# Optimization experiments

Hardware: AMD Instinct MI355X
Metric: run time of the kernel (lower is better)

The kernel has to match this reference:

```python
import jax, jax.numpy as jnp
import numpy as np

FILLER = 10.1  # filler_value from __init__
B, C, L, KEEP = 128, 16, 16384, 12288


def setup_inputs() -> dict:
    key = jax.random.key(0)
    k1, k2, k3, k4 = jax.random.split(key, 4)
    x1 = jax.random.normal(k1, (B, C, 4096), dtype=jnp.float32)
    x2 = jax.random.normal(k2, (B, C, 4096), dtype=jnp.float32)
    x3 = jax.random.normal(k3, (B, C, L), dtype=jnp.float32)
    # Scatter exactly (L - KEEP) filler entries at random positions in every row,
    # so per-row compaction yields a uniform length KEEP (required by np.stack
    # in the original module).
    u = jax.random.uniform(k4, (B, C, L))
    ranks = jnp.argsort(jnp.argsort(u, axis=-1), axis=-1)  # random permutation ranks
    fill_mask = ranks < (L - KEEP)
    x3 = jnp.where(fill_mask, jnp.float32(FILLER), x3)
    return {"x1": x1, "x2": x2, "x3": x3, "keep_len": KEEP}


def reference(x1, x2, x3, keep_len):
    # Per-row stream compaction: drop entries equal to FILLER, keep original
    # order of survivors, output fixed length keep_len.
    is_filler = x3 == jnp.float32(FILLER)          # [B, C, L] bool
    # Stable argsort moves non-filler (False=0) to the front, order-preserving.
    order = jnp.argsort(is_filler, axis=-1, stable=True)  # [B, C, L]
    compacted = jnp.take_along_axis(x3, order, axis=-1)    # [B, C, L]
    return compacted[..., :keep_len]                        # [B, C, keep_len]
```

## Files before the change

### kernel.cpp

```cpp
#include <hip/hip_runtime.h>


#define FILLER_VAL 10.1f
constexpr int L_LEN    = 16384;
constexpr int KEEP_LEN = 12288;
constexpr int BLOCK    = 256;
constexpr int NW       = BLOCK / 64;
constexpr int CHUNK    = BLOCK * 4;
constexpr int NC       = L_LEN / CHUNK;

__global__ __launch_bounds__(BLOCK) void compact_rows_kernel(
    const float* __restrict__ x3, float* __restrict__ out)
{
    const int row = blockIdx.x;
    const float* __restrict__ in = x3 + (size_t)row * L_LEN;
    float* __restrict__ o = out + (size_t)row * KEEP_LEN;

    const int tid  = threadIdx.x;
    const int lane = tid & 63;
    const int wid  = tid >> 6;
    const unsigned long long lt = (1ULL << lane) - 1ULL;

    __shared__ float stage[KEEP_LEN];
    __shared__ int wtot[NC][NW];

    float4 v[NC];
    #pragma unroll
    for (int c = 0; c < NC; ++c)
        v[c] = *reinterpret_cast<const float4*>(in + c * CHUNK + tid * 4);

    int before[NC];
    #pragma unroll
    for (int c = 0; c < NC; ++c) {
        unsigned long long m0 = __ballot(v[c].x != FILLER_VAL);
        unsigned long long m1 = __ballot(v[c].y != FILLER_VAL);
        unsigned long long m2 = __ballot(v[c].z != FILLER_VAL);
        unsigned long long m3 = __ballot(v[c].w != FILLER_VAL);
        before[c] = __popcll(m0 & lt) + __popcll(m1 & lt)
                  + __popcll(m2 & lt) + __popcll(m3 & lt);
        if (lane == 0)
            wtot[c][wid] = __popcll(m0) + __popcll(m1)
                         + __popcll(m2) + __popcll(m3);
    }
    __syncthreads();

    int run = 0;
    #pragma unroll
    for (int c = 0; c < NC; ++c) {
        int wb = run;
        #pragma unroll
        for (int w = 0; w < NW; ++w) {
            int t = wtot[c][w];
            if (w < wid) wb += t;
            run += t;
        }
        int pos = wb + before[c];
        if (v[c].x != FILLER_VAL) { if (pos < KEEP_LEN) stage[pos] = v[c].x; ++pos; }
        if (v[c].y != FILLER_VAL) { if (pos < KEEP_LEN) stage[pos] = v[c].y; ++pos; }
        if (v[c].z != FILLER_VAL) { if (pos < KEEP_LEN) stage[pos] = v[c].z; ++pos; }
        if (v[c].w != FILLER_VAL) { if (pos < KEEP_LEN) stage[pos] = v[c].w; ++pos; }
    }
    __syncthreads();

    #pragma unroll
    for (int k = 0; k < KEEP_LEN / (BLOCK * 4); ++k) {
        const int idx = (k * BLOCK + tid) * 4;
        float4 val = *reinterpret_cast<const float4*>(&stage[idx]);
        *reinterpret_cast<float4*>(&o[idx]) = val;
    }
}

extern "C" void kernel_launch(void* const* d_in, const int* in_sizes, int n_in,
                              void* d_out, int out_size, void* d_ws, size_t ws_size,
                              hipStream_t stream)
{
    const float* x3 = (const float*)d_in[2];
    float* out = (float*)d_out;

    const int rows = in_sizes[2] / L_LEN;

    compact_rows_kernel<<<rows, BLOCK, 0, stream>>>(x3, out);
}
```

Before: 256.4 us.

## Process two rows per 512-thread block with both rows' loads issued upfront

```diff
diff --git a/kernel.cpp b/kernel.cpp
--- a/kernel.cpp
+++ b/kernel.cpp
@@ -4,46 +4,47 @@
 #define FILLER_VAL 10.1f
 constexpr int L_LEN    = 16384;
 constexpr int KEEP_LEN = 12288;
-constexpr int BLOCK    = 256;
+constexpr int BLOCK    = 512;
 constexpr int NW       = BLOCK / 64;
 constexpr int CHUNK    = BLOCK * 4;
 constexpr int NC       = L_LEN / CHUNK;
 
-__global__ __launch_bounds__(BLOCK) void compact_rows_kernel(
-    const float* __restrict__ x3, float* __restrict__ out)
+struct RowState {
+    float4 v[NC];
+    int before[NC];
+    int b0[NC], b1[NC], b2[NC];
+};
+
+__device__ __forceinline__ void load_row(RowState& s, const float* __restrict__ in, int tid)
 {
-    const int row = blockIdx.x;
-    const float* __restrict__ in = x3 + (size_t)row * L_LEN;
-    float* __restrict__ o = out + (size_t)row * KEEP_LEN;
-
-    const int tid  = threadIdx.x;
-    const int lane = tid & 63;
-    const int wid  = tid >> 6;
-    const unsigned long long lt = (1ULL << lane) - 1ULL;
-
-    __shared__ float stage[KEEP_LEN];
-    __shared__ int wtot[NC][NW];
-
-    float4 v[NC];
     #pragma unroll
     for (int c = 0; c < NC; ++c)
-        v[c] = *reinterpret_cast<const float4*>(in + c * CHUNK + tid * 4);
+        s.v[c] = *reinterpret_cast<const float4*>(in + c * CHUNK + tid * 4);
+}
 
-    int before[NC];
+__device__ __forceinline__ void ballot_row(RowState& s, int lane, int wid,
+                                           unsigned long long lt, int (*wtot)[NW])
+{
     #pragma unroll
     for (int c = 0; c < NC; ++c) {
-        unsigned long long m0 = __ballot(v[c].x != FILLER_VAL);
-        unsigned long long m1 = __ballot(v[c].y != FILLER_VAL);
-        unsigned long long m2 = __ballot(v[c].z != FILLER_VAL);
-        unsigned long long m3 = __ballot(v[c].w != FILLER_VAL);
-        before[c] = __popcll(m0 & lt) + __popcll(m1 & lt)
-                  + __popcll(m2 & lt) + __popcll(m3 & lt);
+        unsigned long long m0 = __ballot(s.v[c].x != FILLER_VAL);
+        unsigned long long m1 = __ballot(s.v[c].y != FILLER_VAL);
+        unsigned long long m2 = __ballot(s.v[c].z != FILLER_VAL);
+        unsigned long long m3 = __ballot(s.v[c].w != FILLER_VAL);
+        s.before[c] = __popcll(m0 & lt) + __popcll(m1 & lt)
+                    + __popcll(m2 & lt) + __popcll(m3 & lt);
+        s.b0[c] = (int)((m0 >> lane) & 1ULL);
+        s.b1[c] = (int)((m1 >> lane) & 1ULL);
+        s.b2[c] = (int)((m2 >> lane) & 1ULL);
         if (lane == 0)
             wtot[c][wid] = __popcll(m0) + __popcll(m1)
                          + __popcll(m2) + __popcll(m3);
     }
-    __syncthreads();
+}
 
+__device__ __forceinline__ void scatter_row(const RowState& s, int wid,
+                                            float* stage, const int (*wtot)[NW])
+{
     int run = 0;
     #pragma unroll
     for (int c = 0; c < NC; ++c) {
@@ -54,20 +55,60 @@
             if (w < wid) wb += t;
             run += t;
         }
-        int pos = wb + before[c];
-        if (v[c].x != FILLER_VAL) { if (pos < KEEP_LEN) stage[pos] = v[c].x; ++pos; }
-        if (v[c].y != FILLER_VAL) { if (pos < KEEP_LEN) stage[pos] = v[c].y; ++pos; }
-        if (v[c].z != FILLER_VAL) { if (pos < KEEP_LEN) stage[pos] = v[c].z; ++pos; }
-        if (v[c].w != FILLER_VAL) { if (pos < KEEP_LEN) stage[pos] = v[c].w; ++pos; }
+        const int p0 = wb + s.before[c];
+        const int p1 = p0 + s.b0[c];
+        const int p2 = p1 + s.b1[c];
+        const int p3 = p2 + s.b2[c];
+        if (s.v[c].x != FILLER_VAL && p0 < KEEP_LEN) stage[p0] = s.v[c].x;
+        if (s.v[c].y != FILLER_VAL && p1 < KEEP_LEN) stage[p1] = s.v[c].y;
+        if (s.v[c].z != FILLER_VAL && p2 < KEEP_LEN) stage[p2] = s.v[c].z;
+        if (s.v[c].w != FILLER_VAL && p3 < KEEP_LEN) stage[p3] = s.v[c].w;
     }
-    __syncthreads();
+}
 
+__device__ __forceinline__ void copyout_row(const float* stage, float* __restrict__ o, int tid)
+{
     #pragma unroll
     for (int k = 0; k < KEEP_LEN / (BLOCK * 4); ++k) {
         const int idx = (k * BLOCK + tid) * 4;
-        float4 val = *reinterpret_cast<const float4*>(&stage[idx]);
-        *reinterpret_cast<float4*>(&o[idx]) = val;
+        *reinterpret_cast<float4*>(&o[idx]) =
+            *reinterpret_cast<const float4*>(&stage[idx]);
     }
+}
+
+__global__ __launch_bounds__(BLOCK, 6) void compact_rows_kernel(
+    const float* __restrict__ x3, float* __restrict__ out, int rows)
+{
+    const int row0 = blockIdx.x * 2;
+    const int row1 = row0 + 1;
+    const bool has1 = (row1 < rows);
+
+    const int tid  = threadIdx.x;
+    const int lane = tid & 63;
+    const int wid  = tid >> 6;
+    const unsigned long long lt = (1ULL << lane) - 1ULL;
+
+    __shared__ float stage[KEEP_LEN];
+    __shared__ int wtot[NC][NW];
+
+    RowState s0, s1;
+
+    load_row(s0, x3 + (size_t)row0 * L_LEN, tid);
+    if (has1) load_row(s1, x3 + (size_t)row1 * L_LEN, tid);
+
+    ballot_row(s0, lane, wid, lt, wtot);
+    __syncthreads();
+    scatter_row(s0, wid, stage, wtot);
+    __syncthreads();
+    copyout_row(stage, out + (size_t)row0 * KEEP_LEN, tid);
+
+    if (has1) ballot_row(s1, lane, wid, lt, wtot);
+    __syncthreads();
+    if (has1) {
+        scatter_row(s1, wid, stage, wtot);
+    }
+    __syncthreads();
+    if (has1) copyout_row(stage, out + (size_t)row1 * KEEP_LEN, tid);
 }
 
 extern "C" void kernel_launch(void* const* d_in, const int* in_sizes, int n_in,
@@ -78,6 +119,7 @@
     float* out = (float*)d_out;
 
     const int rows = in_sizes[2] / L_LEN;
+    const int grid = (rows + 1) / 2;
 
-    compact_rows_kernel<<<rows, BLOCK, 0, stream>>>(x3, out);
+    compact_rows_kernel<<<grid, BLOCK, 0, stream>>>(x3, out, rows);
 }
```

Measured after the change: 266.3 us. 3.9% more time.

## Stage 16-bit source indices in LDS and gather values from global memory

Applied to the files above, without the earlier changes.

```diff
diff --git a/kernel.cpp b/kernel.cpp
--- a/kernel.cpp
+++ b/kernel.cpp
@@ -9,7 +9,7 @@
 constexpr int CHUNK    = BLOCK * 4;
 constexpr int NC       = L_LEN / CHUNK;
 
-__global__ __launch_bounds__(BLOCK) void compact_rows_kernel(
+__global__ __launch_bounds__(BLOCK, 6) void compact_rows_kernel(
     const float* __restrict__ x3, float* __restrict__ out)
 {
     const int row = blockIdx.x;
@@ -21,23 +21,24 @@
     const int wid  = tid >> 6;
     const unsigned long long lt = (1ULL << lane) - 1ULL;
 
-    __shared__ float stage[KEEP_LEN];
+    __shared__ unsigned short stage[KEEP_LEN];
     __shared__ int wtot[NC][NW];
 
-    float4 v[NC];
-    #pragma unroll
-    for (int c = 0; c < NC; ++c)
-        v[c] = *reinterpret_cast<const float4*>(in + c * CHUNK + tid * 4);
-
-    int before[NC];
+    int pk[NC];
     #pragma unroll
     for (int c = 0; c < NC; ++c) {
-        unsigned long long m0 = __ballot(v[c].x != FILLER_VAL);
-        unsigned long long m1 = __ballot(v[c].y != FILLER_VAL);
-        unsigned long long m2 = __ballot(v[c].z != FILLER_VAL);
-        unsigned long long m3 = __ballot(v[c].w != FILLER_VAL);
-        before[c] = __popcll(m0 & lt) + __popcll(m1 & lt)
-                  + __popcll(m2 & lt) + __popcll(m3 & lt);
+        const float4 v = *reinterpret_cast<const float4*>(in + c * CHUNK + tid * 4);
+        const unsigned long long m0 = __ballot(v.x != FILLER_VAL);
+        const unsigned long long m1 = __ballot(v.y != FILLER_VAL);
+        const unsigned long long m2 = __ballot(v.z != FILLER_VAL);
+        const unsigned long long m3 = __ballot(v.w != FILLER_VAL);
+        const int before = __popcll(m0 & lt) + __popcll(m1 & lt)
+                         + __popcll(m2 & lt) + __popcll(m3 & lt);
+        const int bits = (int)((m0 >> lane) & 1ULL)
+                       | ((int)((m1 >> lane) & 1ULL) << 1)
+                       | ((int)((m2 >> lane) & 1ULL) << 2)
+                       | ((int)((m3 >> lane) & 1ULL) << 3);
+        pk[c] = bits | (before << 4);
         if (lane == 0)
             wtot[c][wid] = __popcll(m0) + __popcll(m1)
                          + __popcll(m2) + __popcll(m3);
@@ -50,23 +51,35 @@
         int wb = run;
         #pragma unroll
         for (int w = 0; w < NW; ++w) {
-            int t = wtot[c][w];
+            const int t = wtot[c][w];
             if (w < wid) wb += t;
             run += t;
         }
-        int pos = wb + before[c];
-        if (v[c].x != FILLER_VAL) { if (pos < KEEP_LEN) stage[pos] = v[c].x; ++pos; }
-        if (v[c].y != FILLER_VAL) { if (pos < KEEP_LEN) stage[pos] = v[c].y; ++pos; }
-        if (v[c].z != FILLER_VAL) { if (pos < KEEP_LEN) stage[pos] = v[c].z; ++pos; }
-        if (v[c].w != FILLER_VAL) { if (pos < KEEP_LEN) stage[pos] = v[c].w; ++pos; }
+        const int bits   = pk[c] & 15;
+        const int before = pk[c] >> 4;
+        const int p0 = wb + before;
+        const int p1 = p0 + (bits & 1);
+        const int p2 = p1 + ((bits >> 1) & 1);
+        const int p3 = p2 + ((bits >> 2) & 1);
+        const int idx = c * CHUNK + tid * 4;
+        if ((bits & 1) && p0 < KEEP_LEN) stage[p0] = (unsigned short)(idx);
+        if ((bits & 2) && p1 < KEEP_LEN) stage[p1] = (unsigned short)(idx + 1);
+        if ((bits & 4) && p2 < KEEP_LEN) stage[p2] = (unsigned short)(idx + 2);
+        if ((bits & 8) && p3 < KEEP_LEN) stage[p3] = (unsigned short)(idx + 3);
     }
     __syncthreads();
 
     #pragma unroll
-    for (int k = 0; k < KEEP_LEN / (BLOCK * 4); ++k) {
-        const int idx = (k * BLOCK + tid) * 4;
-        float4 val = *reinterpret_cast<const float4*>(&stage[idx]);
-        *reinterpret_cast<float4*>(&o[idx]) = val;
+    for (int it = 0; it < KEEP_LEN / (BLOCK * 8); ++it) {
+        const int o0 = it * (BLOCK * 8) + tid * 4;
+        const int o1 = o0 + BLOCK * 4;
+        const ushort4 i0 = *reinterpret_cast<const ushort4*>(&stage[o0]);
+        const ushort4 i1 = *reinterpret_cast<const ushort4*>(&stage[o1]);
+        float4 a, b;
+        a.x = in[i0.x]; a.y = in[i0.y]; a.z = in[i0.z]; a.w = in[i0.w];
+        b.x = in[i1.x]; b.y = in[i1.y]; b.z = in[i1.z]; b.w = in[i1.w];
+        *reinterpret_cast<float4*>(&o[o0]) = a;
+        *reinterpret_cast<float4*>(&o[o1]) = b;
     }
 }
 
```

New measurement: 272.0 us. 1.06x slower.

## Compact each row with a single wavefront using a streaming LDS ring buffer

Applied to the files above, without the earlier changes.

```diff
diff --git a/kernel.cpp b/kernel.cpp
--- a/kernel.cpp
+++ b/kernel.cpp
@@ -4,69 +4,87 @@
 #define FILLER_VAL 10.1f
 constexpr int L_LEN    = 16384;
 constexpr int KEEP_LEN = 12288;
-constexpr int BLOCK    = 256;
-constexpr int NW       = BLOCK / 64;
-constexpr int CHUNK    = BLOCK * 4;
-constexpr int NC       = L_LEN / CHUNK;
+constexpr int WAVE     = 64;
+constexpr int CHUNK    = WAVE * 4;
+constexpr int CPR      = L_LEN / CHUNK;
+constexpr int PF       = 8;
+constexpr int RING     = 2048;
+constexpr int RM       = RING - 1;
+constexpr int FLUSH_Q  = 256;
 
-__global__ __launch_bounds__(BLOCK) void compact_rows_kernel(
+__device__ __forceinline__ int lane_prefix(unsigned long long m)
+{
+    return __builtin_amdgcn_mbcnt_hi((unsigned)(m >> 32),
+           __builtin_amdgcn_mbcnt_lo((unsigned)m, 0u));
+}
+
+__global__ __launch_bounds__(WAVE, 4) void compact_rows_kernel(
     const float* __restrict__ x3, float* __restrict__ out)
 {
-    const int row = blockIdx.x;
+    const int row  = blockIdx.x;
+    const int lane = threadIdx.x;
     const float* __restrict__ in = x3 + (size_t)row * L_LEN;
     float* __restrict__ o = out + (size_t)row * KEEP_LEN;
 
-    const int tid  = threadIdx.x;
-    const int lane = tid & 63;
-    const int wid  = tid >> 6;
-    const unsigned long long lt = (1ULL << lane) - 1ULL;
+    __shared__ float ring[RING];
 
-    __shared__ float stage[KEEP_LEN];
-    __shared__ int wtot[NC][NW];
+    float4 buf[PF];
+    #pragma unroll
+    for (int i = 0; i < PF; ++i)
+        buf[i] = *reinterpret_cast<const float4*>(in + i * CHUNK + lane * 4);
 
-    float4 v[NC];
+    int rowoff  = 0;
+    int flushed = 0;
+
+    #pragma unroll 1
+    for (int g = 0; g < CPR / PF; ++g) {
+        #pragma unroll
+        for (int s = 0; s < PF; ++s) {
+            const int c = g * PF + s;
+            const float4 v = buf[s];
+            if (c + PF < CPR)
+                buf[s] = *reinterpret_cast<const float4*>(
+                    in + (c + PF) * CHUNK + lane * 4);
+
+            const bool kx = (v.x != FILLER_VAL);
+            const bool ky = (v.y != FILLER_VAL);
+            const bool kz = (v.z != FILLER_VAL);
+            const bool kw = (v.w != FILLER_VAL);
+            const unsigned long long m0 = __ballot(kx);
+            const unsigned long long m1 = __ballot(ky);
+            const unsigned long long m2 = __ballot(kz);
+            const unsigned long long m3 = __ballot(kw);
+
+            const int before = lane_prefix(m0) + lane_prefix(m1)
+                             + lane_prefix(m2) + lane_prefix(m3);
+            const int p0 = rowoff + before;
+            const int p1 = p0 + (int)kx;
+            const int p2 = p1 + (int)ky;
+            const int p3 = p2 + (int)kz;
+            if (kx) ring[p0 & RM] = v.x;
+            if (ky) ring[p1 & RM] = v.y;
+            if (kz) ring[p2 & RM] = v.z;
+            if (kw) ring[p3 & RM] = v.w;
+
+            rowoff += __popcll(m0) + __popcll(m1)
+                    + __popcll(m2) + __popcll(m3);
+
+            while (rowoff - flushed >= FLUSH_Q) {
+                const int rbase = (flushed & RM) + lane * 4;
+                const float4 t = *reinterpret_cast<const float4*>(&ring[rbase]);
+                if (flushed < KEEP_LEN)
+                    *reinterpret_cast<float4*>(&o[flushed + lane * 4]) = t;
+                flushed += FLUSH_Q;
+            }
+        }
+    }
+
+    const int rem = rowoff - flushed;
     #pragma unroll
-    for (int c = 0; c < NC; ++c)
-        v[c] = *reinterpret_cast<const float4*>(in + c * CHUNK + tid * 4);
-
-    int before[NC];
-    #pragma unroll
-    for (int c = 0; c < NC; ++c) {
-        unsigned long long m0 = __ballot(v[c].x != FILLER_VAL);
-        unsigned long long m1 = __ballot(v[c].y != FILLER_VAL);
-        unsigned long long m2 = __ballot(v[c].z != FILLER_VAL);
-        unsigned long long m3 = __ballot(v[c].w != FILLER_VAL);
-        before[c] = __popcll(m0 & lt) + __popcll(m1 & lt)
-                  + __popcll(m2 & lt) + __popcll(m3 & lt);
-        if (lane == 0)
-            wtot[c][wid] = __popcll(m0) + __popcll(m1)
-                         + __popcll(m2) + __popcll(m3);
-    }
-    __syncthreads();
-
-    int run = 0;
-    #pragma unroll
-    for (int c = 0; c < NC; ++c) {
-        int wb = run;
-        #pragma unroll
-        for (int w = 0; w < NW; ++w) {
-            int t = wtot[c][w];
-            if (w < wid) wb += t;
-            run += t;
-        }
-        int pos = wb + before[c];
-        if (v[c].x != FILLER_VAL) { if (pos < KEEP_LEN) stage[pos] = v[c].x; ++pos; }
-        if (v[c].y != FILLER_VAL) { if (pos < KEEP_LEN) stage[pos] = v[c].y; ++pos; }
-        if (v[c].z != FILLER_VAL) { if (pos < KEEP_LEN) stage[pos] = v[c].z; ++pos; }
-        if (v[c].w != FILLER_VAL) { if (pos < KEEP_LEN) stage[pos] = v[c].w; ++pos; }
-    }
-    __syncthreads();
-
-    #pragma unroll
-    for (int k = 0; k < KEEP_LEN / (BLOCK * 4); ++k) {
-        const int idx = (k * BLOCK + tid) * 4;
-        float4 val = *reinterpret_cast<const float4*>(&stage[idx]);
-        *reinterpret_cast<float4*>(&o[idx]) = val;
+    for (int j = 0; j < 4; ++j) {
+        const int i = lane * 4 + j;
+        if (i < rem && flushed + i < KEEP_LEN)
+            o[flushed + i] = ring[(flushed + i) & RM];
     }
 }
 
@@ -79,5 +97,5 @@
 
     const int rows = in_sizes[2] / L_LEN;
 
-    compact_rows_kernel<<<rows, BLOCK, 0, stream>>>(x3, out);
+    compact_rows_kernel<<<rows, WAVE, 0, stream>>>(x3, out);
 }
```

Measured after the change: 256.7 us. Within noise of the previous version (+0.1%).
